# Performance work log

Hardware: AMD Instinct MI355X
Metric: run time of the kernel (lower is better)

## Reference

```python
import jax, jax.numpy as jnp
import numpy as np

STAGES = 3
CAUSAL = True


def sine_positional_encoding(T, D, dtype=jnp.float32):
    # keras_nlp SinePositionEncoding: interleaved sin/cos, base 10000
    pos = jnp.arange(T, dtype=dtype)[:, None]            # [T,1]
    i = jnp.arange(D)[None, :]                            # [1,D]
    angle = pos / jnp.power(jnp.asarray(10000.0, dtype), (2 * (i // 2)).astype(dtype) / D)
    return jnp.where(i % 2 == 0, jnp.sin(angle), jnp.cos(angle))  # [T,D]


def setup_inputs() -> dict:
    key = jax.random.key(0)
    kX, kWp, kbp, kWf, kbf = jax.random.split(key, 5)
    B, T, D = 4, 4096, 1024
    X = jax.random.normal(kX, (B, T, D), dtype=jnp.float32)
    # data_projection: D -> (stages+1)*D
    Wp = jax.random.normal(kWp, (D, (STAGES + 1) * D), dtype=jnp.float32) / np.sqrt(D)
    bp = jnp.zeros(((STAGES + 1) * D,), dtype=jnp.float32)
    # filters: D -> stages*D (applied to positional encoding)
    Wf = jax.random.normal(kWf, (D, STAGES * D), dtype=jnp.float32) / np.sqrt(D)
    bf = jnp.zeros((STAGES * D,), dtype=jnp.float32)
    return {"X": X, "Wp": Wp, "bp": bp, "Wf": Wf, "bf": bf}


def reference(X, Wp, bp, Wf, bf):
    B, T, D = X.shape
    # linear projections of data: [B,T,stages+1,D]
    xp = (jnp.einsum('btd,de->bte', X, Wp) + bp).reshape(B, T, STAGES + 1, D)
    # filters from sinusoidal positional encoding (batch-independent): [T,stages,D]
    pos = sine_positional_encoding(T, D, X.dtype)
    f = (pos @ Wf + bf).reshape(T, STAGES, D)
    if CAUSAL:
        # zero-pad time axis to 2T -> circular FFT conv becomes linear (causal) conv
        xp = jnp.concatenate([xp, jnp.zeros_like(xp)], axis=1)   # [B,2T,S+1,D]
        f = jnp.concatenate([f, jnp.zeros_like(f)], axis=0)      # [2T,S,D]
    L = xp.shape[1]
    F = jnp.fft.rfft(f, axis=0)                                   # [L//2+1,S,D]
    y = xp[:, :, 0, :]                                            # [B,L,D]
    for i in range(STAGES):
        conv = jnp.fft.irfft(jnp.fft.rfft(y, axis=1) * F[None, :, i, :], n=L, axis=1)
        y = conv * xp[:, :, i + 1, :]
    return y[:, :T, :] if CAUSAL else y
```

## Files before the change

### kernel.cpp

```cpp
#include <hip/hip_runtime.h>
#include <math.h>

#define T_LEN 4096
#define D_DIM 1024
#define B_DIM 4
#define N_STAGES 3
#define FT 512

typedef unsigned short bf16_t;
typedef __bf16 bf16x8 __attribute__((ext_vector_type(8)));
typedef float f32x4 __attribute__((ext_vector_type(4)));

#define SW(i) ((i) ^ ((((unsigned)(i)) >> 4) & 15))

__device__ __forceinline__ bf16_t f2bf(float f) {
    union { float f; unsigned u; } v; v.f = f;
    unsigned r = v.u + 0x7FFFu + ((v.u >> 16) & 1u);
    return (bf16_t)(r >> 16);
}
__device__ __forceinline__ float bf2f(bf16_t h) {
    union { unsigned u; float f; } v; v.u = ((unsigned)h) << 16;
    return v.f;
}
__device__ __forceinline__ float2 cmul(float2 a, float2 b) {
    return make_float2(a.x * b.x - a.y * b.y, a.x * b.y + a.y * b.x);
}
__device__ __forceinline__ float2 cadd(float2 a, float2 b) { return make_float2(a.x + b.x, a.y + b.y); }
__device__ __forceinline__ float2 csub(float2 a, float2 b) { return make_float2(a.x - b.x, a.y - b.y); }
__device__ __forceinline__ float2 conjf2(float2 a) { return make_float2(a.x, -a.y); }

#define GLOAD_LDS16(gp, lp) __builtin_amdgcn_global_load_lds( \
    (const __attribute__((address_space(1))) void*)(gp),      \
    (__attribute__((address_space(3))) void*)(lp), 16, 0, 0)

__global__ __launch_bounds__(256) void pos_kernel(bf16_t* __restrict__ posbf) {
    int idx = blockIdx.x * 256 + threadIdx.x;
    int t = idx >> 10;
    int k = idx & 1023;
    float e = (float)(k & ~1) / (float)D_DIM;
    float r = exp2f(-e * 13.287712379549449f);
    float angle = (float)t * r;
    float v = (k & 1) ? cosf(angle) : sinf(angle);
    posbf[idx] = f2bf(v);
}

__global__ __launch_bounds__(256) void f32_to_bf16_kernel(const float* __restrict__ in,
                                                          bf16_t* __restrict__ out, int n8) {
    int i = blockIdx.x * 256 + threadIdx.x;
    if (i >= n8) return;
    float4 a = ((const float4*)in)[i * 2];
    float4 b = ((const float4*)in)[i * 2 + 1];
    ((ushort4*)out)[i * 2]     = make_ushort4(f2bf(a.x), f2bf(a.y), f2bf(a.z), f2bf(a.w));
    ((ushort4*)out)[i * 2 + 1] = make_ushort4(f2bf(b.x), f2bf(b.y), f2bf(b.z), f2bf(b.w));
}

__global__ __launch_bounds__(256) void transpose_to_bf16(const float* __restrict__ in,
                                                         bf16_t* __restrict__ out, int K, int N) {
    __shared__ float tile[32][33];
    const int n0 = blockIdx.x * 32;
    const int k0 = blockIdx.y * 32;
    const int tx = threadIdx.x & 31;
    const int ty = threadIdx.x >> 5;
    for (int i = ty; i < 32; i += 8)
        tile[i][tx] = in[(size_t)(k0 + i) * N + n0 + tx];
    __syncthreads();
    for (int i = ty; i < 32; i += 8)
        out[(size_t)(n0 + i) * K + k0 + tx] = f2bf(tile[tx][i]);
}

template <int MODE>
__global__ __launch_bounds__(256) void mfma_gemm(const bf16_t* __restrict__ A,
                                                 const bf16_t* __restrict__ BT,
                                                 const float* __restrict__ bias,
                                                 void* __restrict__ outv,
                                                 int M, int N, int K, int nbx) {
    constexpr int SMEM_BYTES = (MODE == 0) ? (128 * 136 * 2) : (128 * 132 * 4);
    __shared__ __align__(16) char smem[SMEM_BYTES];
    bf16_t* As = (bf16_t*)smem;
    bf16_t* Bs = (bf16_t*)(smem + 8192);

    const int tid = threadIdx.x;
    const int lane = tid & 63;
    const int w = tid >> 6;
    const int wr = w >> 1, wc = w & 1;

    const int nwg = gridDim.x;
    const int q = nwg >> 3;
    const int swz = (blockIdx.x & 7) * q + (blockIdx.x >> 3);
    const int by = swz / nbx, bx = swz - by * nbx;
    const int row0 = by * 128, col0 = bx * 128;

    f32x4 acc[4][4];
#pragma unroll
    for (int m = 0; m < 4; ++m)
#pragma unroll
        for (int n = 0; n < 4; ++n) acc[m][n] = (f32x4)(0.0f);

    int offs[2], rr[2], kk8[2];
#pragma unroll
    for (int c = 0; c < 2; ++c) {
        offs[c] = (w * 2 + c) * 1024 + lane * 16;
        rr[c] = offs[c] >> 6;
        kk8[c] = ((offs[c] >> 4) & 3) * 8;
    }

    for (int k0 = 0; k0 < K; k0 += 32) {
#pragma unroll
        for (int c = 0; c < 2; ++c) {
            const bf16_t* gA = A + (size_t)(row0 + rr[c]) * K + k0 + kk8[c];
            GLOAD_LDS16(gA, As + (w * 2 + c) * 512);
            const bf16_t* gB = BT + (size_t)(col0 + rr[c]) * K + k0 + kk8[c];
            GLOAD_LDS16(gB, Bs + (w * 2 + c) * 512);
        }
        __syncthreads();

        bf16x8 af[4], bfr[4];
#pragma unroll
        for (int m = 0; m < 4; ++m)
            af[m] = *(const bf16x8*)&As[(wr * 64 + m * 16 + (lane & 15)) * 32 + (lane >> 4) * 8];
#pragma unroll
        for (int n = 0; n < 4; ++n)
            bfr[n] = *(const bf16x8*)&Bs[(wc * 64 + n * 16 + (lane & 15)) * 32 + (lane >> 4) * 8];
#pragma unroll
        for (int m = 0; m < 4; ++m)
#pragma unroll
            for (int n = 0; n < 4; ++n)
                acc[m][n] = __builtin_amdgcn_mfma_f32_16x16x32_bf16(af[m], bfr[n], acc[m][n], 0, 0, 0);
        __syncthreads();
    }

    if (MODE == 0) {
        bf16_t* Cs = (bf16_t*)smem;
#pragma unroll
        for (int m = 0; m < 4; ++m)
#pragma unroll
            for (int n = 0; n < 4; ++n) {
                int cl = wc * 64 + n * 16 + (lane & 15);
                int rlb = wr * 64 + m * 16 + ((lane >> 4) << 2);
                float bb = bias[col0 + cl];
#pragma unroll
                for (int j = 0; j < 4; ++j)
                    Cs[cl * 136 + rlb + j] = f2bf(acc[m][n][j] + bb);
            }
        __syncthreads();
        int dl = tid >> 1, th = tid & 1;
        int cc = col0 + dl;
        int s = cc >> 10, d = cc & 1023;
        int b = row0 >> 12;
        int t0 = (row0 & 4095) + th * 64;
        uint4* dst = (uint4*)&((bf16_t*)outv)[((size_t)(s * 4 + b) * 1024 + d) * 4096 + t0];
        const uint4* src = (const uint4*)&Cs[dl * 136 + th * 64];
#pragma unroll
        for (int j = 0; j < 8; ++j) dst[j] = src[j];
    } else {
        float* CsF = (float*)smem;
#pragma unroll
        for (int m = 0; m < 4; ++m)
#pragma unroll
            for (int n = 0; n < 4; ++n) {
                int cl = wc * 64 + n * 16 + (lane & 15);
                int rlb = wr * 64 + m * 16 + ((lane >> 4) << 2);
                float bb = bias[col0 + cl];
#pragma unroll
                for (int j = 0; j < 4; ++j)
                    CsF[cl * 132 + rlb + j] = acc[m][n][j] + bb;
            }
        __syncthreads();
        int dl = tid >> 1, th = tid & 1;
        int cc = col0 + dl;
        uint4* dst = (uint4*)&((float*)outv)[(size_t)cc * 4096 + row0 + th * 64];
        const uint4* src = (const uint4*)&CsF[dl * 132 + th * 64];
#pragma unroll
        for (int j = 0; j < 16; ++j) dst[j] = src[j];
    }
}

template <int INV>
__device__ __forceinline__ void bfly4(float2& a, float2& b, float2& c, float2& d) {
    float2 t0 = cadd(a, c), t1 = csub(a, c), t2 = cadd(b, d), t3 = csub(b, d);
    float2 it3 = INV ? make_float2(-t3.y, t3.x) : make_float2(t3.y, -t3.x);
    a = cadd(t0, t2); b = cadd(t1, it3); c = csub(t0, t2); d = csub(t1, it3);
}

template <int INV>
__device__ __forceinline__ void dft8(float2 (&x)[8]) {
    bfly4<INV>(x[0], x[2], x[4], x[6]);
    bfly4<INV>(x[1], x[3], x[5], x[7]);
    const float s2 = 0.70710678118654752f;
    const float2 o1 = INV ? make_float2(s2, s2) : make_float2(s2, -s2);
    const float2 o3 = INV ? make_float2(-s2, s2) : make_float2(-s2, -s2);
    x[3] = cmul(x[3], o1);
    x[5] = INV ? make_float2(-x[5].y, x[5].x) : make_float2(x[5].y, -x[5].x);
    x[7] = cmul(x[7], o3);
    float2 F0 = cadd(x[0], x[1]), F4 = csub(x[0], x[1]);
    float2 F1 = cadd(x[2], x[3]), F5 = csub(x[2], x[3]);
    float2 F2 = cadd(x[4], x[5]), F6 = csub(x[4], x[5]);
    float2 F3 = cadd(x[6], x[7]), F7 = csub(x[6], x[7]);
    x[0] = F0; x[1] = F1; x[2] = F2; x[3] = F3;
    x[4] = F4; x[5] = F5; x[6] = F6; x[7] = F7;
}

template <int INV, int M>
__device__ __forceinline__ void r8_pass(float2* __restrict__ s, const float2* __restrict__ Wq) {
    const int p = threadIdx.x;
    const int r = p & (M - 1);
    const int jm = p - r;
    float2 x[8];
#pragma unroll
    for (int c = 0; c < 8; ++c) x[c] = s[SW(p + 512 * c)];
    __syncthreads();
    dft8<INV>(x);
    const int base = 8 * jm + r;
    if (M == 512) {
#pragma unroll
        for (int q = 0; q < 8; ++q) s[SW(base + q * 512)] = x[q];
    } else {
        float2 w1 = Wq[jm];
        if (INV) w1.y = -w1.y;
        float2 w2 = cmul(w1, w1);
        float2 w3 = cmul(w2, w1);
        float2 w4 = cmul(w2, w2);
        s[SW(base)]         = x[0];
        s[SW(base + M)]     = cmul(w1, x[1]);
        s[SW(base + 2 * M)] = cmul(w2, x[2]);
        s[SW(base + 3 * M)] = cmul(w3, x[3]);
        s[SW(base + 4 * M)] = cmul(w4, x[4]);
        s[SW(base + 5 * M)] = cmul(cmul(w4, w1), x[5]);
        s[SW(base + 6 * M)] = cmul(cmul(w4, w2), x[6]);
        s[SW(base + 7 * M)] = cmul(cmul(w4, w3), x[7]);
    }
    __syncthreads();
}

template <int INV>
__device__ __forceinline__ void fft4096_ip(float2* __restrict__ s, const float2* __restrict__ Wq) {
    r8_pass<INV, 1>(s, Wq);
    r8_pass<INV, 8>(s, Wq);
    r8_pass<INV, 64>(s, Wq);
    r8_pass<INV, 512>(s, Wq);
}

template <int INV, int M>
__device__ __forceinline__ void r8_pass4(float2 (*__restrict__ s)[4096],
                                         const float2* __restrict__ Wq) {
    const int p = threadIdx.x;
    const int r = p & (M - 1);
    const int jm = p - r;
    float2 x[4][8];
#pragma unroll
    for (int bb = 0; bb < 4; ++bb)
#pragma unroll
        for (int c = 0; c < 8; ++c) x[bb][c] = s[bb][SW(p + 512 * c)];
    __syncthreads();
    const int base = 8 * jm + r;
    if (M == 512) {
#pragma unroll
        for (int bb = 0; bb < 4; ++bb) {
            dft8<INV>(x[bb]);
#pragma unroll
            for (int q = 0; q < 8; ++q) s[bb][SW(base + q * 512)] = x[bb][q];
        }
    } else {
        float2 w1 = Wq[jm];
        if (INV) w1.y = -w1.y;
        float2 w2 = cmul(w1, w1);
        float2 w3 = cmul(w2, w1);
        float2 w4 = cmul(w2, w2);
        float2 w5 = cmul(w4, w1);
        float2 w6 = cmul(w4, w2);
        float2 w7 = cmul(w4, w3);
#pragma unroll
        for (int bb = 0; bb < 4; ++bb) {
            dft8<INV>(x[bb]);
            s[bb][SW(base)]         = x[bb][0];
            s[bb][SW(base + M)]     = cmul(w1, x[bb][1]);
            s[bb][SW(base + 2 * M)] = cmul(w2, x[bb][2]);
            s[bb][SW(base + 3 * M)] = cmul(w3, x[bb][3]);
            s[bb][SW(base + 4 * M)] = cmul(w4, x[bb][4]);
            s[bb][SW(base + 5 * M)] = cmul(w5, x[bb][5]);
            s[bb][SW(base + 6 * M)] = cmul(w6, x[bb][6]);
            s[bb][SW(base + 7 * M)] = cmul(w7, x[bb][7]);
        }
    }
    __syncthreads();
}

template <int INV>
__device__ __forceinline__ void fft4096_ip4(float2 (*__restrict__ s)[4096],
                                            const float2* __restrict__ Wq) {
    r8_pass4<INV, 1>(s, Wq);
    r8_pass4<INV, 8>(s, Wq);
    r8_pass4<INV, 64>(s, Wq);
    r8_pass4<INV, 512>(s, Wq);
}

__device__ __forceinline__ void init_tables(float2* __restrict__ Wq, float2* __restrict__ Wu) {
    const int tid = threadIdx.x;
    {
        float sn, cs;
        __sincosf((float)tid * -1.5339807878856412e-3f, &sn, &cs);
        Wq[tid] = make_float2(cs, sn);
    }
#pragma unroll
    for (int u = 0; u < 4; ++u) {
        int k = u * FT + tid;
        float sn, cs;
        __sincosf((float)k * -7.669903939428206e-4f, &sn, &cs);
        Wu[k] = make_float2(cs, sn);
    }
}

__device__ __forceinline__ float2 spec_load(const void* spec, int bf, size_t row, int k) {
    if (bf) {
        ushort2 h = ((const ushort2*)spec)[row * 4097 + k];
        return make_float2(bf2f(h.x), bf2f(h.y));
    }
    return ((const float2*)spec)[row * 4097 + k];
}
__device__ __forceinline__ void spec_store(void* spec, int bf, size_t row, int k, float2 v) {
    if (bf) ((ushort2*)spec)[row * 4097 + k] = make_ushort2(f2bf(v.x), f2bf(v.y));
    else    ((float2*)spec)[row * 4097 + k] = v;
}

__global__ __launch_bounds__(FT)
void filter_fft_kernel(const float* __restrict__ fT,
                       void* __restrict__ specv,
                       int spec_bf16) {
    __shared__ __align__(16) float2 sA[4096];
    __shared__ float2 Wq[512];
    __shared__ float2 Wu[2048];
    const int tid = threadIdx.x;
    const size_t row = blockIdx.x;
    init_tables(Wq, Wu);
    const float4* f4 = (const float4*)&fT[row * T_LEN];
#pragma unroll
    for (int u = 0; u < 2; ++u) {
        int j = u * FT + tid;
        float4 v = f4[j];
        sA[SW(2 * j)]     = make_float2(v.x, v.y);
        sA[SW(2 * j + 1)] = make_float2(v.z, v.w);
    }
#pragma unroll
    for (int u = 0; u < 4; ++u) {
        int n = 2048 + u * FT + tid;
        sA[SW(n)] = make_float2(0.0f, 0.0f);
    }
    __syncthreads();
    fft4096_ip<0>(sA, Wq);
#pragma unroll
    for (int u = 0; u < 4; ++u) {
        int s = u * FT + tid;
        if (s < 2047) {
            int k = s + 1, nk = 4096 - k;
            float2 Zk = sA[SW(k)], Zn = sA[SW(nk)];
            float2 Ye = make_float2(0.5f * (Zk.x + Zn.x), 0.5f * (Zk.y - Zn.y));
            float2 Yo = make_float2(0.5f * (Zk.y + Zn.y), -0.5f * (Zk.x - Zn.x));
            float2 w = Wu[k];
            float2 wYo = cmul(w, Yo);
            spec_store(specv, spec_bf16, row, k, cadd(Ye, wYo));
            spec_store(specv, spec_bf16, row, nk, conjf2(csub(Ye, wYo)));
        }
    }
    if (tid == 0) {
        float2 Z0 = sA[SW(0)];
        spec_store(specv, spec_bf16, row, 0,    make_float2(Z0.x + Z0.y, 0.0f));
        spec_store(specv, spec_bf16, row, 4096, make_float2(Z0.x - Z0.y, 0.0f));
        spec_store(specv, spec_bf16, row, 2048, conjf2(sA[SW(2048)]));
    }
}

__global__ __launch_bounds__(FT)
void conv_kernel(const bf16_t* __restrict__ xpT,
                 const void* __restrict__ specv,
                 int spec_bf16,
                 bf16_t* __restrict__ yT) {
    __shared__ __align__(16) float2 sA[4][4096];
    __shared__ float2 Wq[512];
    __shared__ float2 Wu[2048];
    const int tid = threadIdx.x;
    const int d = blockIdx.x;
    init_tables(Wq, Wu);

#pragma unroll
    for (int bb = 0; bb < 4; ++bb) {
        const ushort4* y4 = (const ushort4*)&xpT[((size_t)bb * 1024 + d) * T_LEN];
#pragma unroll
        for (int u = 0; u < 2; ++u) {
            int j = u * FT + tid;
            ushort4 h = y4[j];
            sA[bb][SW(2 * j)]     = make_float2(bf2f(h.x), bf2f(h.y));
            sA[bb][SW(2 * j + 1)] = make_float2(bf2f(h.z), bf2f(h.w));
        }
#pragma unroll
        for (int u = 0; u < 4; ++u) {
            int n = 2048 + u * FT + tid;
            sA[bb][SW(n)] = make_float2(0.0f, 0.0f);
        }
    }
    __syncthreads();

    const float scale = 1.0f / 4096.0f;
    for (int st = 0; st < N_STAGES; ++st) {
        fft4096_ip4<0>(sA, Wq);
        const size_t row = (size_t)st * 1024 + d;
#pragma unroll
        for (int u = 0; u < 4; ++u) {
            int s = u * FT + tid;
            if (s < 2047) {
                int k = s + 1, nk = 4096 - k;
                float2 w = Wu[k];
                float2 cw = conjf2(w);
                float2 Fk = spec_load(specv, spec_bf16, row, k);
                float2 Fn = spec_load(specv, spec_bf16, row, nk);
#pragma unroll
                for (int bb = 0; bb < 4; ++bb) {
                    float2 Zk = sA[bb][SW(k)], Zn = sA[bb][SW(nk)];
                    float2 Ye = make_float2(0.5f * (Zk.x + Zn.x), 0.5f * (Zk.y - Zn.y));
                    float2 Yo = make_float2(0.5f * (Zk.y + Zn.y), -0.5f * (Zk.x - Zn.x));
                    float2 wYo = cmul(w, Yo);
                    float2 Yk = cadd(Ye, wYo);
                    float2 Ynk = conjf2(csub(Ye, wYo));
                    float2 Hk = cmul(Yk, Fk);
                    float2 Hn = cmul(Ynk, Fn);
                    float2 He = make_float2(0.5f * (Hk.x + Hn.x), 0.5f * (Hk.y - Hn.y));
                    float2 Hd = make_float2(0.5f * (Hk.x - Hn.x), 0.5f * (Hk.y + Hn.y));
                    float2 Ho = cmul(cw, Hd);
                    sA[bb][SW(k)]  = make_float2(He.x - Ho.y, He.y + Ho.x);
                    sA[bb][SW(nk)] = make_float2(He.x + Ho.y, Ho.x - He.y);
                }
            }
        }
        if (tid == 0) {
            float2 F0 = spec_load(specv, spec_bf16, row, 0);
            float2 FN = spec_load(specv, spec_bf16, row, 4096);
            float2 F2 = spec_load(specv, spec_bf16, row, 2048);
#pragma unroll
            for (int bb = 0; bb < 4; ++bb) {
                float2 Z0 = sA[bb][SW(0)];
                float Y0 = Z0.x + Z0.y, YN = Z0.x - Z0.y;
                float2 H0 = make_float2(Y0 * F0.x, Y0 * F0.y);
                float2 HN = make_float2(YN * FN.x, YN * FN.y);
                float2 He0 = make_float2(0.5f * (H0.x + HN.x), 0.5f * (H0.y + HN.y));
                float2 Ho0 = make_float2(0.5f * (H0.x - HN.x), 0.5f * (H0.y - HN.y));
                sA[bb][SW(0)] = make_float2(He0.x - Ho0.y, He0.y + Ho0.x);
                float2 H2 = cmul(conjf2(sA[bb][SW(2048)]), F2);
                sA[bb][SW(2048)] = conjf2(H2);
            }
        }
        __syncthreads();
        fft4096_ip4<1>(sA, Wq);

        if (st < N_STAGES - 1) {
#pragma unroll
            for (int bb = 0; bb < 4; ++bb) {
                const ushort4* g4 = (const ushort4*)&xpT[((size_t)((st + 1) * 4 + bb) * 1024 + d) * T_LEN];
#pragma unroll
                for (int u = 0; u < 2; ++u) {
                    int j = u * FT + tid;
                    ushort4 h = g4[j];
                    float2 v0 = sA[bb][SW(2 * j)], v1 = sA[bb][SW(2 * j + 1)];
                    sA[bb][SW(2 * j)]     = make_float2(v0.x * scale * bf2f(h.x), v0.y * scale * bf2f(h.y));
                    sA[bb][SW(2 * j + 1)] = make_float2(v1.x * scale * bf2f(h.z), v1.y * scale * bf2f(h.w));
                }
#pragma unroll
                for (int u = 0; u < 4; ++u) {
                    int n = 2048 + u * FT + tid;
                    sA[bb][SW(n)] = make_float2(0.0f, 0.0f);
                }
            }
            __syncthreads();
        } else {
#pragma unroll
            for (int bb = 0; bb < 4; ++bb) {
                const ushort4* g4 = (const ushort4*)&xpT[((size_t)((st + 1) * 4 + bb) * 1024 + d) * T_LEN];
                ushort4* yrow = (ushort4*)&yT[((size_t)bb * 1024 + d) * T_LEN];
#pragma unroll
                for (int u = 0; u < 2; ++u) {
                    int j = u * FT + tid;
                    ushort4 h = g4[j];
                    float2 v0 = sA[bb][SW(2 * j)], v1 = sA[bb][SW(2 * j + 1)];
                    yrow[j] = make_ushort4(f2bf(v0.x * scale * bf2f(h.x)),
                                           f2bf(v0.y * scale * bf2f(h.y)),
                                           f2bf(v1.x * scale * bf2f(h.z)),
                                           f2bf(v1.y * scale * bf2f(h.w)));
                }
            }
        }
    }
}

__global__ __launch_bounds__(256) void transpose_out(const bf16_t* __restrict__ yT,
                                                     float* __restrict__ out) {
    __shared__ float tile[32][33];
    const int tb = blockIdx.z;
    const int t0 = blockIdx.x * 32;
    const int d0 = blockIdx.y * 32;
    const int tx = threadIdx.x & 31;
    const int ty = threadIdx.x >> 5;
    for (int i = ty; i < 32; i += 8)
        tile[i][tx] = bf2f(yT[((size_t)tb * 1024 + d0 + i) * 4096 + t0 + tx]);
    __syncthreads();
    for (int i = ty; i < 32; i += 8)
        out[((size_t)tb * 4096 + t0 + i) * 1024 + d0 + tx] = tile[tx][i];
}

extern "C" void kernel_launch(void* const* d_in, const int* in_sizes, int n_in,
                              void* d_out, int out_size, void* d_ws, size_t ws_size,
                              hipStream_t stream) {
    const float* X   = (const float*)d_in[0];
    const float* Wp  = (const float*)d_in[1];
    const float* bp  = (const float*)d_in[2];
    const float* Wf  = (const float*)d_in[3];
    const float* bfv = (const float*)d_in[4];
    float* out = (float*)d_out;
    char* ws = (char*)d_ws;

    const size_t XPT_BYTES  = (size_t)134217728;
    const size_t SPEC_F32_B = (size_t)3 * 1024 * 4097 * 8;
    const size_t SPEC_BF_B  = (size_t)3 * 1024 * 4097 * 4;
    const size_t XBF_BYTES  = (size_t)33554432;
    const size_t WPT_BYTES  = (size_t)8388608;

    bf16_t* xpT   = (bf16_t*)ws;
    bf16_t* posbf = (bf16_t*)ws;
    bf16_t* WfT   = (bf16_t*)(ws + 16777216);
    float*  fT    = (float*)(ws + 33554432);
    void*   spec  = (void*)(ws + XPT_BYTES);

    int spec_bf16;
    size_t spec_bytes;
    if (ws_size >= XPT_BYTES + SPEC_F32_B + XBF_BYTES + WPT_BYTES) {
        spec_bf16 = 0; spec_bytes = SPEC_F32_B;
    } else {
        spec_bf16 = 1; spec_bytes = SPEC_BF_B;
    }
    bf16_t* Xbf = (bf16_t*)(ws + XPT_BYTES + spec_bytes);
    bf16_t* WpT = (bf16_t*)(ws + XPT_BYTES + spec_bytes + XBF_BYTES);
    bf16_t* yT  = Xbf;

    pos_kernel<<<(T_LEN * D_DIM) / 256, 256, 0, stream>>>(posbf);

    transpose_to_bf16<<<dim3(3072 / 32, 1024 / 32), 256, 0, stream>>>(Wf, WfT, 1024, 3072);
    mfma_gemm<1><<<768, 256, 0, stream>>>(posbf, WfT, bfv, fT, 4096, 3072, 1024, 24);

    filter_fft_kernel<<<N_STAGES * D_DIM, FT, 0, stream>>>(fT, spec, spec_bf16);

    f32_to_bf16_kernel<<<8192, 256, 0, stream>>>(X, Xbf, 2097152);
    transpose_to_bf16<<<dim3(4096 / 32, 1024 / 32), 256, 0, stream>>>(Wp, WpT, 1024, 4096);
    mfma_gemm<0><<<4096, 256, 0, stream>>>(Xbf, WpT, bp, xpT, 16384, 4096, 1024, 32);

    conv_kernel<<<D_DIM, FT, 0, stream>>>(xpT, spec, spec_bf16, yT);

    transpose_out<<<dim3(4096 / 32, 1024 / 32, B_DIM), 256, 0, stream>>>(yT, out);
}
```

Baseline: 683.2 us.

## Run conv FFTs with 1024 threads, two batches per half-block, padded LDS

The conv kernel now launches 1024 threads per block. Each half of the block runs the radix-8 FFT passes for two of the four batch rows, instead of 512 threads handling all four. This cuts per-thread register pressure from 32 to 16 complex values and doubles the threads available to hide latency. The XOR swizzle on LDS indices is replaced with padding (4 float2 every 64 entries), which slightly enlarges shared memory and changes the bank-conflict pattern.

```diff
diff --git a/kernel.cpp b/kernel.cpp
--- a/kernel.cpp
+++ b/kernel.cpp
@@ -6,12 +6,14 @@
 #define B_DIM 4
 #define N_STAGES 3
 #define FT 512
+#define CT 1024
 
 typedef unsigned short bf16_t;
 typedef __bf16 bf16x8 __attribute__((ext_vector_type(8)));
 typedef float f32x4 __attribute__((ext_vector_type(4)));
 
-#define SW(i) ((i) ^ ((((unsigned)(i)) >> 4) & 15))
+#define PD(i) ((i) + ((((unsigned)(i)) >> 6) << 2))
+#define PADN 4352
 
 __device__ __forceinline__ bf16_t f2bf(float f) {
     union { float f; unsigned u; } v; v.f = f;
@@ -207,27 +209,27 @@
     const int jm = p - r;
     float2 x[8];
 #pragma unroll
-    for (int c = 0; c < 8; ++c) x[c] = s[SW(p + 512 * c)];
+    for (int c = 0; c < 8; ++c) x[c] = s[PD(p + 512 * c)];
     __syncthreads();
     dft8<INV>(x);
     const int base = 8 * jm + r;
     if (M == 512) {
 #pragma unroll
-        for (int q = 0; q < 8; ++q) s[SW(base + q * 512)] = x[q];
+        for (int q = 0; q < 8; ++q) s[PD(base + q * 512)] = x[q];
     } else {
         float2 w1 = Wq[jm];
         if (INV) w1.y = -w1.y;
         float2 w2 = cmul(w1, w1);
         float2 w3 = cmul(w2, w1);
         float2 w4 = cmul(w2, w2);
-        s[SW(base)]         = x[0];
-        s[SW(base + M)]     = cmul(w1, x[1]);
-        s[SW(base + 2 * M)] = cmul(w2, x[2]);
-        s[SW(base + 3 * M)] = cmul(w3, x[3]);
-        s[SW(base + 4 * M)] = cmul(w4, x[4]);
-        s[SW(base + 5 * M)] = cmul(cmul(w4, w1), x[5]);
-        s[SW(base + 6 * M)] = cmul(cmul(w4, w2), x[6]);
-        s[SW(base + 7 * M)] = cmul(cmul(w4, w3), x[7]);
+        s[PD(base)]         = x[0];
+        s[PD(base + M)]     = cmul(w1, x[1]);
+        s[PD(base + 2 * M)] = cmul(w2, x[2]);
+        s[PD(base + 3 * M)] = cmul(w3, x[3]);
+        s[PD(base + 4 * M)] = cmul(w4, x[4]);
+        s[PD(base + 5 * M)] = cmul(cmul(w4, w1), x[5]);
+        s[PD(base + 6 * M)] = cmul(cmul(w4, w2), x[6]);
+        s[PD(base + 7 * M)] = cmul(cmul(w4, w3), x[7]);
     }
     __syncthreads();
 }
@@ -241,24 +243,25 @@
 }
 
 template <int INV, int M>
-__device__ __forceinline__ void r8_pass4(float2 (*__restrict__ s)[4096],
+__device__ __forceinline__ void r8_pass2(float2 (*__restrict__ s)[PADN],
                                          const float2* __restrict__ Wq) {
-    const int p = threadIdx.x;
+    const int p = threadIdx.x & 511;
+    const int sb = (threadIdx.x >> 9) << 1;
     const int r = p & (M - 1);
     const int jm = p - r;
-    float2 x[4][8];
-#pragma unroll
-    for (int bb = 0; bb < 4; ++bb)
-#pragma unroll
-        for (int c = 0; c < 8; ++c) x[bb][c] = s[bb][SW(p + 512 * c)];
+    float2 x[2][8];
+#pragma unroll
+    for (int e = 0; e < 2; ++e)
+#pragma unroll
+        for (int c = 0; c < 8; ++c) x[e][c] = s[sb + e][PD(p + 512 * c)];
     __syncthreads();
     const int base = 8 * jm + r;
     if (M == 512) {
 #pragma unroll
-        for (int bb = 0; bb < 4; ++bb) {
-            dft8<INV>(x[bb]);
-#pragma unroll
-            for (int q = 0; q < 8; ++q) s[bb][SW(base + q * 512)] = x[bb][q];
+        for (int e = 0; e < 2; ++e) {
+            dft8<INV>(x[e]);
+#pragma unroll
+            for (int q = 0; q < 8; ++q) s[sb + e][PD(base + q * 512)] = x[e][q];
         }
     } else {
         float2 w1 = Wq[jm];
@@ -270,40 +273,41 @@
         float2 w6 = cmul(w4, w2);
         float2 w7 = cmul(w4, w3);
 #pragma unroll
-        for (int bb = 0; bb < 4; ++bb) {
-            dft8<INV>(x[bb]);
-            s[bb][SW(base)]         = x[bb][0];
-            s[bb][SW(base + M)]     = cmul(w1, x[bb][1]);
-            s[bb][SW(base + 2 * M)] = cmul(w2, x[bb][2]);
-            s[bb][SW(base + 3 * M)] = cmul(w3, x[bb][3]);
-            s[bb][SW(base + 4 * M)] = cmul(w4, x[bb][4]);
-            s[bb][SW(base + 5 * M)] = cmul(w5, x[bb][5]);
-            s[bb][SW(base + 6 * M)] = cmul(w6, x[bb][6]);
-            s[bb][SW(base + 7 * M)] = cmul(w7, x[bb][7]);
+        for (int e = 0; e < 2; ++e) {
+            dft8<INV>(x[e]);
+            s[sb + e][PD(base)]         = x[e][0];
+            s[sb + e][PD(base + M)]     = cmul(w1, x[e][1]);
+            s[sb + e][PD(base + 2 * M)] = cmul(w2, x[e][2]);
+            s[sb + e][PD(base + 3 * M)] = cmul(w3, x[e][3]);
+            s[sb + e][PD(base + 4 * M)] = cmul(w4, x[e][4]);
+            s[sb + e][PD(base + 5 * M)] = cmul(w5, x[e][5]);
+            s[sb + e][PD(base + 6 * M)] = cmul(w6, x[e][6]);
+            s[sb + e][PD(base + 7 * M)] = cmul(w7, x[e][7]);
         }
     }
     __syncthreads();
 }
 
 template <int INV>
-__device__ __forceinline__ void fft4096_ip4(float2 (*__restrict__ s)[4096],
+__device__ __forceinline__ void fft4096_ip2(float2 (*__restrict__ s)[PADN],
                                             const float2* __restrict__ Wq) {
-    r8_pass4<INV, 1>(s, Wq);
-    r8_pass4<INV, 8>(s, Wq);
-    r8_pass4<INV, 64>(s, Wq);
-    r8_pass4<INV, 512>(s, Wq);
-}
-
+    r8_pass2<INV, 1>(s, Wq);
+    r8_pass2<INV, 8>(s, Wq);
+    r8_pass2<INV, 64>(s, Wq);
+    r8_pass2<INV, 512>(s, Wq);
+}
+
+template <int NTHR>
 __device__ __forceinline__ void init_tables(float2* __restrict__ Wq, float2* __restrict__ Wu) {
     const int tid = threadIdx.x;
-    {
+    if (NTHR > 512 ? (tid < 512) : true) {
         float sn, cs;
         __sincosf((float)tid * -1.5339807878856412e-3f, &sn, &cs);
         Wq[tid] = make_float2(cs, sn);
     }
 #pragma unroll
-    for (int u = 0; u < 4; ++u) {
-        int k = u * FT + tid;
+    for (int u = 0; u < 2048 / NTHR; ++u) {
+        int k = u * NTHR + tid;
         float sn, cs;
         __sincosf((float)k * -7.669903939428206e-4f, &sn, &cs);
         Wu[k] = make_float2(cs, sn);
@@ -326,24 +330,24 @@
 void filter_fft_kernel(const float* __restrict__ fT,
                        void* __restrict__ specv,
                        int spec_bf16) {
-    __shared__ __align__(16) float2 sA[4096];
+    __shared__ __align__(16) float2 sA[PADN];
     __shared__ float2 Wq[512];
     __shared__ float2 Wu[2048];
     const int tid = threadIdx.x;
     const size_t row = blockIdx.x;
-    init_tables(Wq, Wu);
+    init_tables<FT>(Wq, Wu);
     const float4* f4 = (const float4*)&fT[row * T_LEN];
 #pragma unroll
     for (int u = 0; u < 2; ++u) {
         int j = u * FT + tid;
         float4 v = f4[j];
-        sA[SW(2 * j)]     = make_float2(v.x, v.y);
-        sA[SW(2 * j + 1)] = make_float2(v.z, v.w);
+        sA[PD(2 * j)]     = make_float2(v.x, v.y);
+        sA[PD(2 * j + 1)] = make_float2(v.z, v.w);
     }
 #pragma unroll
     for (int u = 0; u < 4; ++u) {
         int n = 2048 + u * FT + tid;
-        sA[SW(n)] = make_float2(0.0f, 0.0f);
+        sA[PD(n)] = make_float2(0.0f, 0.0f);
     }
     __syncthreads();
     fft4096_ip<0>(sA, Wq);
@@ -352,7 +356,7 @@
         int s = u * FT + tid;
         if (s < 2047) {
             int k = s + 1, nk = 4096 - k;
-            float2 Zk = sA[SW(k)], Zn = sA[SW(nk)];
+            float2 Zk = sA[PD(k)], Zn = sA[PD(nk)];
             float2 Ye = make_float2(0.5f * (Zk.x + Zn.x), 0.5f * (Zk.y - Zn.y));
             float2 Yo = make_float2(0.5f * (Zk.y + Zn.y), -0.5f * (Zk.x - Zn.x));
             float2 w = Wu[k];
@@ -362,50 +366,49 @@
         }
     }
     if (tid == 0) {
-        float2 Z0 = sA[SW(0)];
+        float2 Z0 = sA[PD(0)];
         spec_store(specv, spec_bf16, row, 0,    make_float2(Z0.x + Z0.y, 0.0f));
         spec_store(specv, spec_bf16, row, 4096, make_float2(Z0.x - Z0.y, 0.0f));
-        spec_store(specv, spec_bf16, row, 2048, conjf2(sA[SW(2048)]));
-    }
-}
-
-__global__ __launch_bounds__(FT)
+        spec_store(specv, spec_bf16, row, 2048, conjf2(sA[PD(2048)]));
+    }
+}
+
+__global__ __launch_bounds__(CT)
 void conv_kernel(const bf16_t* __restrict__ xpT,
                  const void* __restrict__ specv,
                  int spec_bf16,
                  bf16_t* __restrict__ yT) {
-    __shared__ __align__(16) float2 sA[4][4096];
+    __shared__ __align__(16) float2 sA[4][PADN];
     __shared__ float2 Wq[512];
     __shared__ float2 Wu[2048];
     const int tid = threadIdx.x;
     const int d = blockIdx.x;
-    init_tables(Wq, Wu);
+    init_tables<CT>(Wq, Wu);
 
 #pragma unroll
     for (int bb = 0; bb < 4; ++bb) {
         const ushort4* y4 = (const ushort4*)&xpT[((size_t)bb * 1024 + d) * T_LEN];
+        {
+            int j = tid;
+            ushort4 h = y4[j];
+            sA[bb][PD(2 * j)]     = make_float2(bf2f(h.x), bf2f(h.y));
+            sA[bb][PD(2 * j + 1)] = make_float2(bf2f(h.z), bf2f(h.w));
+        }
 #pragma unroll
         for (int u = 0; u < 2; ++u) {
-            int j = u * FT + tid;
-            ushort4 h = y4[j];
-            sA[bb][SW(2 * j)]     = make_float2(bf2f(h.x), bf2f(h.y));
-            sA[bb][SW(2 * j + 1)] = make_float2(bf2f(h.z), bf2f(h.w));
-        }
-#pragma unroll
-        for (int u = 0; u < 4; ++u) {
-            int n = 2048 + u * FT + tid;
-            sA[bb][SW(n)] = make_float2(0.0f, 0.0f);
+            int n = 2048 + u * CT + tid;
+            sA[bb][PD(n)] = make_float2(0.0f, 0.0f);
         }
     }
     __syncthreads();
 
     const float scale = 1.0f / 4096.0f;
     for (int st = 0; st < N_STAGES; ++st) {
-        fft4096_ip4<0>(sA, Wq);
+        fft4096_ip2<0>(sA, Wq);
         const size_t row = (size_t)st * 1024 + d;
 #pragma unroll
-        for (int u = 0; u < 4; ++u) {
-            int s = u * FT + tid;
+        for (int u = 0; u < 2; ++u) {
+            int s = u * CT + tid;
             if (s < 2047) {
                 int k = s + 1, nk = 4096 - k;
                 float2 w = Wu[k];
@@ -414,7 +417,7 @@
                 float2 Fn = spec_load(specv, spec_bf16, row, nk);
 #pragma unroll
                 for (int bb = 0; bb < 4; ++bb) {
-                    float2 Zk = sA[bb][SW(k)], Zn = sA[bb][SW(nk)];
+                    float2 Zk = sA[bb][PD(k)], Zn = sA[bb][PD(nk)];
                     float2 Ye = make_float2(0.5f * (Zk.x + Zn.x), 0.5f * (Zk.y - Zn.y));
                     float2 Yo = make_float2(0.5f * (Zk.y + Zn.y), -0.5f * (Zk.x - Zn.x));
                     float2 wYo = cmul(w, Yo);
@@ -425,8 +428,8 @@
                     float2 He = make_float2(0.5f * (Hk.x + Hn.x), 0.5f * (Hk.y - Hn.y));
                     float2 Hd = make_float2(0.5f * (Hk.x - Hn.x), 0.5f * (Hk.y + Hn.y));
                     float2 Ho = cmul(cw, Hd);
-                    sA[bb][SW(k)]  = make_float2(He.x - Ho.y, He.y + Ho.x);
-                    sA[bb][SW(nk)] = make_float2(He.x + Ho.y, Ho.x - He.y);
+                    sA[bb][PD(k)]  = make_float2(He.x - Ho.y, He.y + Ho.x);
+                    sA[bb][PD(nk)] = make_float2(He.x + Ho.y, Ho.x - He.y);
                 }
             }
         }
@@ -436,36 +439,35 @@
             float2 F2 = spec_load(specv, spec_bf16, row, 2048);
 #pragma unroll
             for (int bb = 0; bb < 4; ++bb) {
-                float2 Z0 = sA[bb][SW(0)];
+                float2 Z0 = sA[bb][PD(0)];
                 float Y0 = Z0.x + Z0.y, YN = Z0.x - Z0.y;
                 float2 H0 = make_float2(Y0 * F0.x, Y0 * F0.y);
                 float2 HN = make_float2(YN * FN.x, YN * FN.y);
                 float2 He0 = make_float2(0.5f * (H0.x + HN.x), 0.5f * (H0.y + HN.y));
                 float2 Ho0 = make_float2(0.5f * (H0.x - HN.x), 0.5f * (H0.y - HN.y));
-                sA[bb][SW(0)] = make_float2(He0.x - Ho0.y, He0.y + Ho0.x);
-                float2 H2 = cmul(conjf2(sA[bb][SW(2048)]), F2);
-                sA[bb][SW(2048)] = conjf2(H2);
+                sA[bb][PD(0)] = make_float2(He0.x - Ho0.y, He0.y + Ho0.x);
+                float2 H2 = cmul(conjf2(sA[bb][PD(2048)]), F2);
+                sA[bb][PD(2048)] = conjf2(H2);
             }
         }
         __syncthreads();
-        fft4096_ip4<1>(sA, Wq);
+        fft4096_ip2<1>(sA, Wq);
 
         if (st < N_STAGES - 1) {
 #pragma unroll
             for (int bb = 0; bb < 4; ++bb) {
                 const ushort4* g4 = (const ushort4*)&xpT[((size_t)((st + 1) * 4 + bb) * 1024 + d) * T_LEN];
+                {
+                    int j = tid;
+                    ushort4 h = g4[j];
+                    float2 v0 = sA[bb][PD(2 * j)], v1 = sA[bb][PD(2 * j + 1)];
+                    sA[bb][PD(2 * j)]     = make_float2(v0.x * scale * bf2f(h.x), v0.y * scale * bf2f(h.y));
+                    sA[bb][PD(2 * j + 1)] = make_float2(v1.x * scale * bf2f(h.z), v1.y * scale * bf2f(h.w));
+                }
 #pragma unroll
                 for (int u = 0; u < 2; ++u) {
-                    int j = u * FT + tid;
-                    ushort4 h = g4[j];
-                    float2 v0 = sA[bb][SW(2 * j)], v1 = sA[bb][SW(2 * j + 1)];
-                    sA[bb][SW(2 * j)]     = make_float2(v0.x * scale * bf2f(h.x), v0.y * scale * bf2f(h.y));
-                    sA[bb][SW(2 * j + 1)] = make_float2(v1.x * scale * bf2f(h.z), v1.y * scale * bf2f(h.w));
-                }
-#pragma unroll
-                for (int u = 0; u < 4; ++u) {
-                    int n = 2048 + u * FT + tid;
-                    sA[bb][SW(n)] = make_float2(0.0f, 0.0f);
+                    int n = 2048 + u * CT + tid;
+                    sA[bb][PD(n)] = make_float2(0.0f, 0.0f);
                 }
             }
             __syncthreads();
@@ -474,16 +476,13 @@
             for (int bb = 0; bb < 4; ++bb) {
                 const ushort4* g4 = (const ushort4*)&xpT[((size_t)((st + 1) * 4 + bb) * 1024 + d) * T_LEN];
                 ushort4* yrow = (ushort4*)&yT[((size_t)bb * 1024 + d) * T_LEN];
-#pragma unroll
-                for (int u = 0; u < 2; ++u) {
-                    int j = u * FT + tid;
-                    ushort4 h = g4[j];
-                    float2 v0 = sA[bb][SW(2 * j)], v1 = sA[bb][SW(2 * j + 1)];
-                    yrow[j] = make_ushort4(f2bf(v0.x * scale * bf2f(h.x)),
-                                           f2bf(v0.y * scale * bf2f(h.y)),
-                                           f2bf(v1.x * scale * bf2f(h.z)),
-                                           f2bf(v1.y * scale * bf2f(h.w)));
-                }
+                int j = tid;
+                ushort4 h = g4[j];
+                float2 v0 = sA[bb][PD(2 * j)], v1 = sA[bb][PD(2 * j + 1)];
+                yrow[j] = make_ushort4(f2bf(v0.x * scale * bf2f(h.x)),
+                                       f2bf(v0.y * scale * bf2f(h.y)),
+                                       f2bf(v1.x * scale * bf2f(h.z)),
+                                       f2bf(v1.y * scale * bf2f(h.w)));
             }
         }
     }
@@ -549,7 +548,7 @@
     transpose_to_bf16<<<dim3(4096 / 32, 1024 / 32), 256, 0, stream>>>(Wp, WpT, 1024, 4096);
     mfma_gemm<0><<<4096, 256, 0, stream>>>(Xbf, WpT, bp, xpT, 16384, 4096, 1024, 32);
 
-    conv_kernel<<<D_DIM, FT, 0, stream>>>(xpT, spec, spec_bf16, yT);
+    conv_kernel<<<D_DIM, CT, 0, stream>>>(xpT, spec, spec_bf16, yT);
 
     transpose_out<<<dim3(4096 / 32, 1024 / 32, B_DIM), 256, 0, stream>>>(yT, out);
 }
```

New measurement: 691.3 us. Within noise of the previous version (+1.2%).
